# Kernel tuning notes

Measured on AMD Instinct MI355X. Metric: run time of the kernel, lower is better.

Reference implementation:

```python
import jax, jax.numpy as jnp
import numpy as np


def gcn_conv(h, src, dst, n, W, b):
    # PyG GCNConv: linear, add self-loops, symmetric norm, scatter-sum, bias
    h = h @ W
    loop = jnp.arange(n)
    s = jnp.concatenate([src, loop])
    d = jnp.concatenate([dst, loop])
    deg = jax.ops.segment_sum(jnp.ones_like(d, h.dtype), d, num_segments=n)
    dinv = jnp.where(deg > 0, jax.lax.rsqrt(deg), 0.0)
    norm = dinv[s] * dinv[d]  # [E+N]
    out = jax.ops.segment_sum(h[s] * norm[:, None], d, num_segments=n)
    return out + b


def setup_inputs() -> dict:
    key = jax.random.key(0)
    ks = jax.random.split(key, 4)
    N, E, F_IN, F_H, F_OUT = 10000, 320000, 512, 128, 40
    x = jax.random.normal(ks[0], (N, F_IN), dtype=jnp.float32)
    edge_index = jax.random.randint(ks[1], (2, E), 0, N, dtype=jnp.int64)
    W1 = jax.random.normal(ks[2], (F_IN, F_H), dtype=jnp.float32) * (1.0 / np.sqrt(F_IN))
    b1 = jnp.zeros((F_H,), jnp.float32)
    W2 = jax.random.normal(ks[3], (F_H, F_OUT), dtype=jnp.float32) * (1.0 / np.sqrt(F_H))
    b2 = jnp.zeros((F_OUT,), jnp.float32)
    return {"x": x, "edge_index": edge_index, "W1": W1, "b1": b1, "W2": W2, "b2": b2}


def reference(x, edge_index, W1, b1, W2, b2):
    n = x.shape[0]
    src, dst = edge_index[0], edge_index[1]
    h = jax.nn.relu(gcn_conv(x, src, dst, n, W1, b1))
    logits = gcn_conv(h, src, dst, n, W2, b2)
    # regularizer: dense adjacency from edge list (duplicates summed), trace(L @ L)
    A = jnp.zeros((n, n), jnp.float32).at[src, dst].add(1.0)
    reg_loss = jnp.sum(A * A.T)  # == trace(A @ A)
    return jax.nn.log_softmax(logits, axis=1), reg_loss
```

## Files before the change

kernel.cpp:

```cpp
#include <hip/hip_runtime.h>
#include <hip/hip_bf16.h>


#define CAP 128

typedef __attribute__((ext_vector_type(8))) short short8;
typedef __attribute__((ext_vector_type(4))) float float4v;

__device__ __forceinline__ unsigned short f2bf(float f) {
    __hip_bfloat16 b = __float2bfloat16(f);
    return *reinterpret_cast<unsigned short*>(&b);
}
__device__ __forceinline__ float bf2f(unsigned short u) {
    __hip_bfloat16 b = *reinterpret_cast<__hip_bfloat16*>(&u);
    return __bfloat162float(b);
}

__global__ void k_prep(const float* __restrict__ x, unsigned short* __restrict__ xh, int total4,
                       const float* __restrict__ W1, unsigned short* __restrict__ Bh1,
                       unsigned short* __restrict__ Bl1,
                       const float* __restrict__ W2, unsigned short* __restrict__ Bh2,
                       unsigned short* __restrict__ Bl2,
                       int* __restrict__ zbase, int zints,
                       int convB, int p1B, int p2B) {
    int b = blockIdx.x;
    if (b < convB) {
        int i = b * 256 + threadIdx.x;
        if (i < total4) {
            float4 v = ((const float4*)x)[i];
            ushort4 h;
            h.x = f2bf(v.x); h.y = f2bf(v.y); h.z = f2bf(v.z); h.w = f2bf(v.w);
            ((ushort4*)xh)[i] = h;
        }
        return;
    }
    b -= convB;
    if (b < p1B) {
        int t = b * 256 + threadIdx.x;
        int lane = t & 63;
        int f = (t >> 6) % 8;
        int kb = (t >> 6) / 8;
        int kbase = kb * 32 + (lane >> 4) * 8;
        int n = f * 16 + (lane & 15);
        unsigned short hj[8], lj[8];
#pragma unroll
        for (int j = 0; j < 8; j++) {
            float v = W1[(size_t)(kbase + j) * 128 + n];
            unsigned short hb = f2bf(v);
            hj[j] = hb;
            lj[j] = f2bf(v - bf2f(hb));
        }
        ushort4 h0 = {hj[0], hj[1], hj[2], hj[3]}, h1 = {hj[4], hj[5], hj[6], hj[7]};
        ushort4 l0 = {lj[0], lj[1], lj[2], lj[3]}, l1 = {lj[4], lj[5], lj[6], lj[7]};
        ((ushort4*)Bh1)[t * 2] = h0; ((ushort4*)Bh1)[t * 2 + 1] = h1;
        ((ushort4*)Bl1)[t * 2] = l0; ((ushort4*)Bl1)[t * 2 + 1] = l1;
        return;
    }
    b -= p1B;
    if (b < p2B) {
        int t = b * 256 + threadIdx.x;
        if (t >= 4 * 3 * 64) return;
        int lane = t & 63;
        int f = (t >> 6) % 3;
        int kb = (t >> 6) / 3;
        int kbase = kb * 32 + (lane >> 4) * 8;
        int n = f * 16 + (lane & 15);
        unsigned short hj[8], lj[8];
#pragma unroll
        for (int j = 0; j < 8; j++) {
            float v = (n < 40) ? W2[(size_t)(kbase + j) * 40 + n] : 0.f;
            unsigned short hb = f2bf(v);
            hj[j] = hb;
            lj[j] = f2bf(v - bf2f(hb));
        }
        ushort4 h0 = {hj[0], hj[1], hj[2], hj[3]}, h1 = {hj[4], hj[5], hj[6], hj[7]};
        ushort4 l0 = {lj[0], lj[1], lj[2], lj[3]}, l1 = {lj[4], lj[5], lj[6], lj[7]};
        ((ushort4*)Bh2)[t * 2] = h0; ((ushort4*)Bh2)[t * 2 + 1] = h1;
        ((ushort4*)Bl2)[t * 2] = l0; ((ushort4*)Bl2)[t * 2 + 1] = l1;
        return;
    }
    b -= p2B;
    {
        int i = b * 256 + threadIdx.x;
        if (i < zints) zbase[i] = 0;
    }
}

__global__ void k_fill(const int* __restrict__ src, const int* __restrict__ dst, int E,
                       int* __restrict__ cnt, unsigned short* __restrict__ csr) {
    int e = blockIdx.x * blockDim.x + threadIdx.x;
    if (e >= E) return;
    int d = dst[e];
    int pos = atomicAdd(&cnt[d], 1);
    if (pos < CAP) csr[(size_t)d * CAP + pos] = (unsigned short)src[e];
}

template <int NF, int KB>
__global__ void k_mfma_gemm1(const unsigned short* __restrict__ Xh,
                             const unsigned short* __restrict__ Bh,
                             const unsigned short* __restrict__ Bl,
                             unsigned short* __restrict__ H0, int M) {
    const int K = KB * 32, N = NF * 16;
    int w = threadIdx.x >> 6, lane = threadIdx.x & 63;
    int m0 = blockIdx.x * 64 + w * 16;
    if (m0 >= M) return;
    float4v acc[NF] = {};
    const short8* A = (const short8*)(Xh + (size_t)(m0 + (lane & 15)) * K) + (lane >> 4);
    const short8* BH = ((const short8*)Bh) + lane;
    const short8* BL = ((const short8*)Bl) + lane;
    for (int kb = 0; kb < KB; kb++) {
        short8 a = A[kb * 4];
#pragma unroll
        for (int f = 0; f < NF; f++) {
            short8 bh = BH[(kb * NF + f) * 64];
            short8 bl = BL[(kb * NF + f) * 64];
            acc[f] = __builtin_amdgcn_mfma_f32_16x16x32_bf16(a, bh, acc[f], 0, 0, 0);
            acc[f] = __builtin_amdgcn_mfma_f32_16x16x32_bf16(a, bl, acc[f], 0, 0, 0);
        }
    }
    int row = (lane >> 4) * 4, col = lane & 15;
#pragma unroll
    for (int f = 0; f < NF; f++)
#pragma unroll
        for (int r = 0; r < 4; r++)
            H0[(size_t)(m0 + row + r) * N + f * 16 + col] = f2bf(acc[f][r]);
}

template <int NF, int KB>
__global__ void k_mfma_gemm2(const unsigned short* __restrict__ Ab,
                             const unsigned short* __restrict__ Bh,
                             const unsigned short* __restrict__ Bl,
                             float* __restrict__ LG, int M) {
    const int K = KB * 32, N = NF * 16;
    int w = threadIdx.x >> 6, lane = threadIdx.x & 63;
    int m0 = blockIdx.x * 64 + w * 16;
    if (m0 >= M) return;
    float4v acc[NF] = {};
    const short8* A = (const short8*)(Ab + (size_t)(m0 + (lane & 15)) * K) + (lane >> 4);
    const short8* BH = ((const short8*)Bh) + lane;
    const short8* BL = ((const short8*)Bl) + lane;
#pragma unroll
    for (int kb = 0; kb < KB; kb++) {
        short8 a = A[kb * 4];
#pragma unroll
        for (int f = 0; f < NF; f++) {
            short8 bh = BH[(kb * NF + f) * 64];
            short8 bl = BL[(kb * NF + f) * 64];
            acc[f] = __builtin_amdgcn_mfma_f32_16x16x32_bf16(a, bh, acc[f], 0, 0, 0);
            acc[f] = __builtin_amdgcn_mfma_f32_16x16x32_bf16(a, bl, acc[f], 0, 0, 0);
        }
    }
    int row = (lane >> 4) * 4, col = lane & 15;
#pragma unroll
    for (int f = 0; f < NF; f++)
#pragma unroll
        for (int r = 0; r < 4; r++)
            LG[(size_t)(m0 + row + r) * N + f * 16 + col] = acc[f][r];
}

__global__ void k_agg1_reg(const int* __restrict__ cnt, const unsigned short* __restrict__ csr,
                           const unsigned short* __restrict__ H, const float* __restrict__ b1,
                           unsigned* __restrict__ aggb,
                           const int* __restrict__ src, const int* __restrict__ dst, int E,
                           float* __restrict__ regp, int Nn, int aggBlocks) {
    if ((int)blockIdx.x < aggBlocks) {
        int wid = blockIdx.x * 4 + (threadIdx.x >> 6);
        int lane = threadIdx.x & 63;
        if (wid >= Nn) return;
        int len = min(cnt[wid], CAP);
        float dd = rsqrtf((float)len + 1.0f);
        const unsigned* H2 = (const unsigned*)H;
        unsigned ph = H2[(size_t)wid * 64 + lane];
        float sw = dd * dd;
        float accx = bf2f((unsigned short)(ph & 0xffff)) * sw;
        float accy = bf2f((unsigned short)(ph >> 16)) * sw;
        const unsigned short* row = csr + (size_t)wid * CAP;
        int j = 0;
        for (; j + 3 < len; j += 4) {
            int s0 = row[j], s1 = row[j + 1], s2 = row[j + 2], s3 = row[j + 3];
            float w0 = rsqrtf((float)cnt[s0] + 1.0f) * dd;
            float w1 = rsqrtf((float)cnt[s1] + 1.0f) * dd;
            float w2 = rsqrtf((float)cnt[s2] + 1.0f) * dd;
            float w3 = rsqrtf((float)cnt[s3] + 1.0f) * dd;
            unsigned p0 = H2[(size_t)s0 * 64 + lane];
            unsigned p1 = H2[(size_t)s1 * 64 + lane];
            unsigned p2 = H2[(size_t)s2 * 64 + lane];
            unsigned p3 = H2[(size_t)s3 * 64 + lane];
            accx += w0 * bf2f((unsigned short)(p0 & 0xffff)) + w1 * bf2f((unsigned short)(p1 & 0xffff));
            accy += w0 * bf2f((unsigned short)(p0 >> 16))   + w1 * bf2f((unsigned short)(p1 >> 16));
            accx += w2 * bf2f((unsigned short)(p2 & 0xffff)) + w3 * bf2f((unsigned short)(p3 & 0xffff));
            accy += w2 * bf2f((unsigned short)(p2 >> 16))   + w3 * bf2f((unsigned short)(p3 >> 16));
        }
        for (; j < len; j++) {
            int s0 = row[j];
            float w0 = rsqrtf((float)cnt[s0] + 1.0f) * dd;
            unsigned p0 = H2[(size_t)s0 * 64 + lane];
            accx += w0 * bf2f((unsigned short)(p0 & 0xffff));
            accy += w0 * bf2f((unsigned short)(p0 >> 16));
        }
        float2 bb = ((const float2*)b1)[lane];
        float vx = accx + bb.x, vy = accy + bb.y;
        vx = vx > 0.f ? vx : 0.f;
        vy = vy > 0.f ? vy : 0.f;
        aggb[(size_t)wid * 64 + lane] = (unsigned)f2bf(vx) | ((unsigned)f2bf(vy) << 16);
    } else {
        int e = ((int)blockIdx.x - aggBlocks) * 256 + (int)threadIdx.x;
        int c = 0;
        if (e < E) {
            int s = src[e];
            unsigned d = (unsigned)dst[e];
            int len = min(cnt[s], CAP);
            const unsigned short* row = csr + (size_t)s * CAP;
            for (int i = 0; i < len; i += 4) {
                uint2 v = *(const uint2*)(row + i);
                c += ((v.x & 0xffffu) == d) ? 1 : 0;
                c += ((v.x >> 16) == d && i + 1 < len) ? 1 : 0;
                c += ((v.y & 0xffffu) == d && i + 2 < len) ? 1 : 0;
                c += ((v.y >> 16) == d && i + 3 < len) ? 1 : 0;
            }
        }
#pragma unroll
        for (int off = 32; off; off >>= 1) c += __shfl_xor(c, off, 64);
        if ((threadIdx.x & 63) == 0 && c) atomicAdd(regp, (float)c);
    }
}

__global__ void k_agg2_lsm(const int* __restrict__ cnt, const unsigned short* __restrict__ csr,
                           const float* __restrict__ LG, const float* __restrict__ b2,
                           const float* __restrict__ regp, float* __restrict__ out,
                           int Nn, int F) {
    int wid = (blockIdx.x * blockDim.x + threadIdx.x) >> 6;
    int lane = threadIdx.x & 63;
    if (wid >= Nn) return;
    int len = min(cnt[wid], CAP);
    float dd = rsqrtf((float)len + 1.0f);
    bool act = lane < F;
    float acc = act ? LG[(size_t)wid * 48 + lane] * dd * dd : 0.f;
    const unsigned short* row = csr + (size_t)wid * CAP;
    int j = 0;
    for (; j + 3 < len; j += 4) {
        int s0 = row[j], s1 = row[j + 1], s2 = row[j + 2], s3 = row[j + 3];
        float w0 = rsqrtf((float)cnt[s0] + 1.0f) * dd;
        float w1 = rsqrtf((float)cnt[s1] + 1.0f) * dd;
        float w2 = rsqrtf((float)cnt[s2] + 1.0f) * dd;
        float w3 = rsqrtf((float)cnt[s3] + 1.0f) * dd;
        float a0 = act ? LG[(size_t)s0 * 48 + lane] : 0.f;
        float a1 = act ? LG[(size_t)s1 * 48 + lane] : 0.f;
        float a2 = act ? LG[(size_t)s2 * 48 + lane] : 0.f;
        float a3 = act ? LG[(size_t)s3 * 48 + lane] : 0.f;
        acc += w0 * a0 + w1 * a1 + w2 * a2 + w3 * a3;
    }
    for (; j < len; j++) {
        int s0 = row[j];
        float w0 = rsqrtf((float)cnt[s0] + 1.0f) * dd;
        float a0 = act ? LG[(size_t)s0 * 48 + lane] : 0.f;
        acc += w0 * a0;
    }
    float v = act ? acc + b2[lane] : -1e30f;
    float m = v;
#pragma unroll
    for (int off = 32; off; off >>= 1) m = fmaxf(m, __shfl_xor(m, off, 64));
    float ex = act ? expf(v - m) : 0.f;
    float ssum = ex;
#pragma unroll
    for (int off = 32; off; off >>= 1) ssum += __shfl_xor(ssum, off, 64);
    if (act) out[(size_t)wid * F + lane] = v - m - logf(ssum);
    if (wid == 0 && lane == 0) out[(size_t)Nn * F] = regp[0];
}

extern "C" void kernel_launch(void* const* d_in, const int* in_sizes, int n_in,
                              void* d_out, int out_size, void* d_ws, size_t ws_size,
                              hipStream_t stream) {
    const float* x  = (const float*)d_in[0];
    const int*   ei = (const int*)d_in[1];
    const float* W1 = (const float*)d_in[2];
    const float* b1 = (const float*)d_in[3];
    const float* W2 = (const float*)d_in[4];
    const float* b2 = (const float*)d_in[5];
    float* out = (float*)d_out;

    const int FH   = in_sizes[3];
    const int FOUT = in_sizes[5];
    const int FIN  = in_sizes[2] / FH;
    const int Nn   = in_sizes[0] / FIN;
    const int E    = in_sizes[1] / 2;
    const int* src = ei;
    const int* dst = ei + E;

    int*   cnt  = (int*)d_ws;
    float* regp = (float*)(cnt + Nn);
    unsigned short* csr   = (unsigned short*)(regp + 16);
    unsigned short* Xh    = csr + (size_t)Nn * CAP;
    unsigned short* H0b   = Xh + (size_t)Nn * FIN;
    unsigned short* AGG1b = H0b + (size_t)Nn * FH;
    unsigned short* Bh1   = AGG1b + (size_t)Nn * FH;
    unsigned short* Bl1   = Bh1 + 65536;
    unsigned short* Bh2   = Bl1 + 65536;
    unsigned short* Bl2   = Bh2 + 6144;
    float* LG0 = (float*)(Bl2 + 6144);

    int total4 = Nn * FIN / 4;
    int convB = (total4 + 255) / 256;
    int p1B = (16 * 8 * 64) / 256;
    int p2B = (4 * 3 * 64 + 255) / 256;
    int zints = Nn + 16;
    int zB = (zints + 255) / 256;
    k_prep<<<convB + p1B + p2B + zB, 256, 0, stream>>>(
        x, Xh, total4, W1, Bh1, Bl1, W2, Bh2, Bl2, cnt, zints, convB, p1B, p2B);

    k_fill<<<(E + 255) / 256, 256, 0, stream>>>(src, dst, E, cnt, csr);

    k_mfma_gemm1<8, 16><<<(Nn + 63) / 64, 256, 0, stream>>>(Xh, Bh1, Bl1, H0b, Nn);

    int aggBlocks = (Nn + 3) / 4;
    int regBlocks = (E + 255) / 256;
    k_agg1_reg<<<aggBlocks + regBlocks, 256, 0, stream>>>(
        cnt, csr, H0b, b1, (unsigned*)AGG1b, src, dst, E, regp, Nn, aggBlocks);

    k_mfma_gemm2<3, 4><<<(Nn + 63) / 64, 256, 0, stream>>>(AGG1b, Bh2, Bl2, LG0, Nn);

    k_agg2_lsm<<<(Nn * 64 + 255) / 256, 256, 0, stream>>>(cnt, csr, LG0, b2, regp, out, Nn, FOUT);
}
```

Before: 201.3 us.

## Precompute degree inverses, widen CSR index loads, store layer-2 logits in bf16

Computes per-node inverse sqrt degree once in extra blocks of the first GEMM launch and reads it in both aggregation kernels instead of recomputing rsqrt from counts per edge. Aggregation loops now load eight neighbour indices with one 16-byte load and unroll by eight for more memory-level parallelism. The second GEMM writes logits in bf16, halving gather traffic in the final aggregation at some precision cost. The regularizer scan also reads eight indices per iteration.

```diff
diff --git a/kernel.cpp b/kernel.cpp
--- a/kernel.cpp
+++ b/kernel.cpp
@@ -99,7 +99,14 @@
 __global__ void k_mfma_gemm1(const unsigned short* __restrict__ Xh,
                              const unsigned short* __restrict__ Bh,
                              const unsigned short* __restrict__ Bl,
-                             unsigned short* __restrict__ H0, int M) {
+                             unsigned short* __restrict__ H0, int M,
+                             const int* __restrict__ cnt, float* __restrict__ dinvf,
+                             int gemmBlocks) {
+    if ((int)blockIdx.x >= gemmBlocks) {
+        int i = ((int)blockIdx.x - gemmBlocks) * 256 + (int)threadIdx.x;
+        if (i < M) dinvf[i] = rsqrtf((float)min(cnt[i], CAP) + 1.0f);
+        return;
+    }
     const int K = KB * 32, N = NF * 16;
     int w = threadIdx.x >> 6, lane = threadIdx.x & 63;
     int m0 = blockIdx.x * 64 + w * 16;
@@ -130,7 +137,7 @@
 __global__ void k_mfma_gemm2(const unsigned short* __restrict__ Ab,
                              const unsigned short* __restrict__ Bh,
                              const unsigned short* __restrict__ Bl,
-                             float* __restrict__ LG, int M) {
+                             unsigned short* __restrict__ LGb, int M) {
     const int K = KB * 32, N = NF * 16;
     int w = threadIdx.x >> 6, lane = threadIdx.x & 63;
     int m0 = blockIdx.x * 64 + w * 16;
@@ -155,10 +162,11 @@
     for (int f = 0; f < NF; f++)
 #pragma unroll
         for (int r = 0; r < 4; r++)
-            LG[(size_t)(m0 + row + r) * N + f * 16 + col] = acc[f][r];
+            LGb[(size_t)(m0 + row + r) * N + f * 16 + col] = f2bf(acc[f][r]);
 }
 
 __global__ void k_agg1_reg(const int* __restrict__ cnt, const unsigned short* __restrict__ csr,
+                           const float* __restrict__ dinvf,
                            const unsigned short* __restrict__ H, const float* __restrict__ b1,
                            unsigned* __restrict__ aggb,
                            const int* __restrict__ src, const int* __restrict__ dst, int E,
@@ -168,7 +176,7 @@
         int lane = threadIdx.x & 63;
         if (wid >= Nn) return;
         int len = min(cnt[wid], CAP);
-        float dd = rsqrtf((float)len + 1.0f);
+        float dd = dinvf[wid];
         const unsigned* H2 = (const unsigned*)H;
         unsigned ph = H2[(size_t)wid * 64 + lane];
         float sw = dd * dd;
@@ -176,24 +184,36 @@
         float accy = bf2f((unsigned short)(ph >> 16)) * sw;
         const unsigned short* row = csr + (size_t)wid * CAP;
         int j = 0;
-        for (; j + 3 < len; j += 4) {
-            int s0 = row[j], s1 = row[j + 1], s2 = row[j + 2], s3 = row[j + 3];
-            float w0 = rsqrtf((float)cnt[s0] + 1.0f) * dd;
-            float w1 = rsqrtf((float)cnt[s1] + 1.0f) * dd;
-            float w2 = rsqrtf((float)cnt[s2] + 1.0f) * dd;
-            float w3 = rsqrtf((float)cnt[s3] + 1.0f) * dd;
+        for (; j + 8 <= len; j += 8) {
+            uint4 idv = *(const uint4*)(row + j);
+            int s0 = idv.x & 0xffff, s1 = idv.x >> 16;
+            int s2 = idv.y & 0xffff, s3 = idv.y >> 16;
+            int s4 = idv.z & 0xffff, s5 = idv.z >> 16;
+            int s6 = idv.w & 0xffff, s7 = idv.w >> 16;
+            float w0 = dinvf[s0], w1 = dinvf[s1], w2 = dinvf[s2], w3 = dinvf[s3];
+            float w4 = dinvf[s4], w5 = dinvf[s5], w6 = dinvf[s6], w7 = dinvf[s7];
             unsigned p0 = H2[(size_t)s0 * 64 + lane];
             unsigned p1 = H2[(size_t)s1 * 64 + lane];
             unsigned p2 = H2[(size_t)s2 * 64 + lane];
             unsigned p3 = H2[(size_t)s3 * 64 + lane];
-            accx += w0 * bf2f((unsigned short)(p0 & 0xffff)) + w1 * bf2f((unsigned short)(p1 & 0xffff));
-            accy += w0 * bf2f((unsigned short)(p0 >> 16))   + w1 * bf2f((unsigned short)(p1 >> 16));
-            accx += w2 * bf2f((unsigned short)(p2 & 0xffff)) + w3 * bf2f((unsigned short)(p3 & 0xffff));
-            accy += w2 * bf2f((unsigned short)(p2 >> 16))   + w3 * bf2f((unsigned short)(p3 >> 16));
+            unsigned p4 = H2[(size_t)s4 * 64 + lane];
+            unsigned p5 = H2[(size_t)s5 * 64 + lane];
+            unsigned p6 = H2[(size_t)s6 * 64 + lane];
+            unsigned p7 = H2[(size_t)s7 * 64 + lane];
+            w0 *= dd; w1 *= dd; w2 *= dd; w3 *= dd;
+            w4 *= dd; w5 *= dd; w6 *= dd; w7 *= dd;
+            accx += w0 * bf2f((unsigned short)(p0 & 0xffff)) + w1 * bf2f((unsigned short)(p1 & 0xffff))
+                  + w2 * bf2f((unsigned short)(p2 & 0xffff)) + w3 * bf2f((unsigned short)(p3 & 0xffff))
+                  + w4 * bf2f((unsigned short)(p4 & 0xffff)) + w5 * bf2f((unsigned short)(p5 & 0xffff))
+                  + w6 * bf2f((unsigned short)(p6 & 0xffff)) + w7 * bf2f((unsigned short)(p7 & 0xffff));
+            accy += w0 * bf2f((unsigned short)(p0 >> 16)) + w1 * bf2f((unsigned short)(p1 >> 16))
+                  + w2 * bf2f((unsigned short)(p2 >> 16)) + w3 * bf2f((unsigned short)(p3 >> 16))
+                  + w4 * bf2f((unsigned short)(p4 >> 16)) + w5 * bf2f((unsigned short)(p5 >> 16))
+                  + w6 * bf2f((unsigned short)(p6 >> 16)) + w7 * bf2f((unsigned short)(p7 >> 16));
         }
         for (; j < len; j++) {
             int s0 = row[j];
-            float w0 = rsqrtf((float)cnt[s0] + 1.0f) * dd;
+            float w0 = dinvf[s0] * dd;
             unsigned p0 = H2[(size_t)s0 * 64 + lane];
             accx += w0 * bf2f((unsigned short)(p0 & 0xffff));
             accy += w0 * bf2f((unsigned short)(p0 >> 16));
@@ -211,12 +231,16 @@
             unsigned d = (unsigned)dst[e];
             int len = min(cnt[s], CAP);
             const unsigned short* row = csr + (size_t)s * CAP;
-            for (int i = 0; i < len; i += 4) {
-                uint2 v = *(const uint2*)(row + i);
+            for (int i = 0; i < len; i += 8) {
+                uint4 v = *(const uint4*)(row + i);
                 c += ((v.x & 0xffffu) == d) ? 1 : 0;
                 c += ((v.x >> 16) == d && i + 1 < len) ? 1 : 0;
                 c += ((v.y & 0xffffu) == d && i + 2 < len) ? 1 : 0;
                 c += ((v.y >> 16) == d && i + 3 < len) ? 1 : 0;
+                c += ((v.z & 0xffffu) == d && i + 4 < len) ? 1 : 0;
+                c += ((v.z >> 16) == d && i + 5 < len) ? 1 : 0;
+                c += ((v.w & 0xffffu) == d && i + 6 < len) ? 1 : 0;
+                c += ((v.w >> 16) == d && i + 7 < len) ? 1 : 0;
             }
         }
 #pragma unroll
@@ -226,34 +250,42 @@
 }
 
 __global__ void k_agg2_lsm(const int* __restrict__ cnt, const unsigned short* __restrict__ csr,
-                           const float* __restrict__ LG, const float* __restrict__ b2,
+                           const float* __restrict__ dinvf,
+                           const unsigned short* __restrict__ LGb, const float* __restrict__ b2,
                            const float* __restrict__ regp, float* __restrict__ out,
                            int Nn, int F) {
     int wid = (blockIdx.x * blockDim.x + threadIdx.x) >> 6;
     int lane = threadIdx.x & 63;
     if (wid >= Nn) return;
     int len = min(cnt[wid], CAP);
-    float dd = rsqrtf((float)len + 1.0f);
+    float dd = dinvf[wid];
     bool act = lane < F;
-    float acc = act ? LG[(size_t)wid * 48 + lane] * dd * dd : 0.f;
+    float acc = act ? bf2f(LGb[(size_t)wid * 48 + lane]) * dd * dd : 0.f;
     const unsigned short* row = csr + (size_t)wid * CAP;
     int j = 0;
-    for (; j + 3 < len; j += 4) {
-        int s0 = row[j], s1 = row[j + 1], s2 = row[j + 2], s3 = row[j + 3];
-        float w0 = rsqrtf((float)cnt[s0] + 1.0f) * dd;
-        float w1 = rsqrtf((float)cnt[s1] + 1.0f) * dd;
-        float w2 = rsqrtf((float)cnt[s2] + 1.0f) * dd;
-        float w3 = rsqrtf((float)cnt[s3] + 1.0f) * dd;
-        float a0 = act ? LG[(size_t)s0 * 48 + lane] : 0.f;
-        float a1 = act ? LG[(size_t)s1 * 48 + lane] : 0.f;
-        float a2 = act ? LG[(size_t)s2 * 48 + lane] : 0.f;
-        float a3 = act ? LG[(size_t)s3 * 48 + lane] : 0.f;
-        acc += w0 * a0 + w1 * a1 + w2 * a2 + w3 * a3;
+    for (; j + 8 <= len; j += 8) {
+        uint4 idv = *(const uint4*)(row + j);
+        int s0 = idv.x & 0xffff, s1 = idv.x >> 16;
+        int s2 = idv.y & 0xffff, s3 = idv.y >> 16;
+        int s4 = idv.z & 0xffff, s5 = idv.z >> 16;
+        int s6 = idv.w & 0xffff, s7 = idv.w >> 16;
+        float w0 = dinvf[s0], w1 = dinvf[s1], w2 = dinvf[s2], w3 = dinvf[s3];
+        float w4 = dinvf[s4], w5 = dinvf[s5], w6 = dinvf[s6], w7 = dinvf[s7];
+        float a0 = act ? bf2f(LGb[(size_t)s0 * 48 + lane]) : 0.f;
+        float a1 = act ? bf2f(LGb[(size_t)s1 * 48 + lane]) : 0.f;
+        float a2 = act ? bf2f(LGb[(size_t)s2 * 48 + lane]) : 0.f;
+        float a3 = act ? bf2f(LGb[(size_t)s3 * 48 + lane]) : 0.f;
+        float a4 = act ? bf2f(LGb[(size_t)s4 * 48 + lane]) : 0.f;
+        float a5 = act ? bf2f(LGb[(size_t)s5 * 48 + lane]) : 0.f;
+        float a6 = act ? bf2f(LGb[(size_t)s6 * 48 + lane]) : 0.f;
+        float a7 = act ? bf2f(LGb[(size_t)s7 * 48 + lane]) : 0.f;
+        acc += (w0 * dd) * a0 + (w1 * dd) * a1 + (w2 * dd) * a2 + (w3 * dd) * a3
+             + (w4 * dd) * a4 + (w5 * dd) * a5 + (w6 * dd) * a6 + (w7 * dd) * a7;
     }
     for (; j < len; j++) {
         int s0 = row[j];
-        float w0 = rsqrtf((float)cnt[s0] + 1.0f) * dd;
-        float a0 = act ? LG[(size_t)s0 * 48 + lane] : 0.f;
+        float w0 = dinvf[s0] * dd;
+        float a0 = act ? bf2f(LGb[(size_t)s0 * 48 + lane]) : 0.f;
         acc += w0 * a0;
     }
     float v = act ? acc + b2[lane] : -1e30f;
@@ -297,7 +329,8 @@
     unsigned short* Bl1   = Bh1 + 65536;
     unsigned short* Bh2   = Bl1 + 65536;
     unsigned short* Bl2   = Bh2 + 6144;
-    float* LG0 = (float*)(Bl2 + 6144);
+    float* dinvf = (float*)(Bl2 + 6144);
+    unsigned short* LGb = (unsigned short*)(dinvf + Nn);
 
     int total4 = Nn * FIN / 4;
     int convB = (total4 + 255) / 256;
@@ -310,14 +343,18 @@
 
     k_fill<<<(E + 255) / 256, 256, 0, stream>>>(src, dst, E, cnt, csr);
 
-    k_mfma_gemm1<8, 16><<<(Nn + 63) / 64, 256, 0, stream>>>(Xh, Bh1, Bl1, H0b, Nn);
+    int gemmB = (Nn + 63) / 64;
+    int dinvB = (Nn + 255) / 256;
+    k_mfma_gemm1<8, 16><<<gemmB + dinvB, 256, 0, stream>>>(
+        Xh, Bh1, Bl1, H0b, Nn, cnt, dinvf, gemmB);
 
     int aggBlocks = (Nn + 3) / 4;
     int regBlocks = (E + 255) / 256;
     k_agg1_reg<<<aggBlocks + regBlocks, 256, 0, stream>>>(
-        cnt, csr, H0b, b1, (unsigned*)AGG1b, src, dst, E, regp, Nn, aggBlocks);
-
-    k_mfma_gemm2<3, 4><<<(Nn + 63) / 64, 256, 0, stream>>>(AGG1b, Bh2, Bl2, LG0, Nn);
-
-    k_agg2_lsm<<<(Nn * 64 + 255) / 256, 256, 0, stream>>>(cnt, csr, LG0, b2, regp, out, Nn, FOUT);
-}
+        cnt, csr, dinvf, H0b, b1, (unsigned*)AGG1b, src, dst, E, regp, Nn, aggBlocks);
+
+    k_mfma_gemm2<3, 4><<<(Nn + 63) / 64, 256, 0, stream>>>(AGG1b, Bh2, Bl2, LGb, Nn);
+
+    k_agg2_lsm<<<(Nn * 64 + 255) / 256, 256, 0, stream>>>(
+        cnt, csr, dinvf, LGb, b2, regp, out, Nn, FOUT);
+}
```

Result: faster. 194.9 us (-3.2%).
